# Optimization experiments

Hardware: AMD Instinct MI355X
Metric: run time of the kernel (lower is better)

Reference implementation:

```python
import jax, jax.numpy as jnp
import numpy as np
import math

# ---------- real Clebsch-Gordan coupling tables (computed once, tiny) ----------
def _cg(j1, m1, j2, m2, j3, m3):
    if m1 + m2 != m3 or j3 < abs(j1 - j2) or j3 > j1 + j2:
        return 0.0
    f = math.factorial
    pre = ((2 * j3 + 1) * f(j3 + j1 - j2) * f(j3 - j1 + j2) * f(j1 + j2 - j3) / f(j1 + j2 + j3 + 1)) ** 0.5
    pre *= (f(j3 + m3) * f(j3 - m3) * f(j1 - m1) * f(j1 + m1) * f(j2 - m2) * f(j2 + m2)) ** 0.5
    s = 0.0
    for k in range(0, j1 + j2 - j3 + 1):
        d = (k, j1 + j2 - j3 - k, j1 - m1 - k, j2 + m2 - k, j3 - j2 + m1 + k, j3 - j1 - m2 + k)
        if min(d) < 0:
            continue
        den = 1
        for t in d:
            den *= f(t)
        s += (-1) ** k / den
    return pre * s

def _Q(l):  # complex->real spherical-harmonic change of basis
    Q = np.zeros((2 * l + 1, 2 * l + 1), dtype=complex)
    Q[l, l] = 1.0
    s = 2 ** -0.5
    for m in range(1, l + 1):
        Q[l + m, l + m] = (-1) ** m * s
        Q[l + m, l - m] = s
        Q[l - m, l + m] = -1j * (-1) ** m * s
        Q[l - m, l - m] = 1j * s
    return Q

def _K(l1, l2, l3):  # real coupling tensor [2l3+1, 2l1+1, 2l2+1]
    C = np.zeros((2 * l3 + 1, 2 * l1 + 1, 2 * l2 + 1), dtype=complex)
    for M3 in range(-l3, l3 + 1):
        for M1 in range(-l1, l1 + 1):
            for M2 in range(-l2, l2 + 1):
                C[M3 + l3, M1 + l1, M2 + l2] = _cg(l1, M1, l2, M2, l3, M3)
    K = np.einsum('cC,aA,bB,CAB->cab', _Q(l3).conj(), _Q(l1), _Q(l2), C)
    K = K.imag if np.abs(K.imag).max() > np.abs(K.real).max() else K.real
    return np.asarray(K, dtype=np.float32)

# the 9 'uvu' instructions (in_l, edge_l, out_l) with multiplicities (weight_numel=144)
_PATHS = [(0, 0, 0), (0, 2, 2), (1, 0, 1), (1, 2, 1), (1, 2, 2), (2, 0, 2), (2, 2, 0), (2, 2, 1), (2, 2, 2)]
_KT = [jnp.asarray(_K(*p)) for p in _PATHS]
_MULS = [32, 32, 16, 16, 16, 8, 8, 8, 8]
_SPLITS = np.cumsum(_MULS)[:-1].tolist()
NEI = 8
EPS = 1e-5

def _sh(u):  # component-normalized real SH of unit vectors, l=0..2 (m order -l..l, l=1 -> y,z,x)
    x, y, z = u[:, 0], u[:, 1], u[:, 2]
    sh0 = jnp.ones_like(x)[:, None]
    sh1 = np.float32(3 ** 0.5) * jnp.stack([y, z, x], -1)
    s15 = np.float32(15 ** 0.5)
    s5 = np.float32(5 ** 0.5)
    sh2 = jnp.stack([s15 * x * y, s15 * y * z, 0.5 * s5 * (3 * z * z - 1.0), s15 * x * z, 0.5 * s15 * (x * x - y * y)], -1)
    return sh0, sh1, sh2

def _path(xs, sh, wp, Kt):  # xs [E,u,2l1+1], sh [E,2l2+1], Kt [2l3+1,2l1+1,2l2+1] -> [E,u,2l3+1]
    return jnp.einsum('eui,ej,oij->euo', xs, sh, Kt) * wp[None, :, None]

def _layer(x0, x1, x2, pos, src, dst, w, W0, W1, W2, bw0, bb0, bw1, bw2, N):
    ev = pos[dst] - pos[src]
    u = ev / (jnp.linalg.norm(ev, axis=1, keepdims=True) + 1e-12)
    sh0, sh1, sh2 = _sh(u)
    s0 = x0[src][:, :, None]  # [E,32,1]
    s1 = x1[src]              # [E,16,3]
    s2 = x2[src]              # [E,8,5]
    ws = jnp.split(w, _SPLITS)
    p1 = _path(s0, sh0, ws[0], _KT[0])
    p2 = _path(s0, sh2, ws[1], _KT[1])
    p3 = _path(s1, sh0, ws[2], _KT[2])
    p4 = _path(s1, sh2, ws[3], _KT[3])
    p5 = _path(s1, sh2, ws[4], _KT[4])
    p6 = _path(s2, sh0, ws[5], _KT[5])
    p7 = _path(s2, sh2, ws[6], _KT[6])
    p8 = _path(s2, sh2, ws[7], _KT[7])
    p9 = _path(s2, sh2, ws[8], _KT[8])
    m0 = jnp.concatenate([p1, p7], 1)          # [E,40,1]
    m1 = jnp.concatenate([p3, p4, p8], 1)      # [E,40,3]
    m2 = jnp.concatenate([p2, p5, p6, p9], 1)  # [E,64,5]
    a0 = jax.ops.segment_sum(m0, dst, num_segments=N)
    a1 = jax.ops.segment_sum(m1, dst, num_segments=N)
    a2 = jax.ops.segment_sum(m2, dst, num_segments=N)
    y0 = (a0[:, :, 0] @ W0) * np.float32(1.0 / 40 ** 0.5)
    y1 = jnp.einsum('num,uv->nvm', a1, W1) * np.float32(1.0 / 40 ** 0.5)
    y2 = jnp.einsum('num,uv->nvm', a2, W2) * np.float32(1.0 / 64 ** 0.5)
    # equivariant batchnorm (training stats): scalars -> standard BN, l>0 -> norm BN
    f = y0 - y0.mean(0)
    y0 = f / jnp.sqrt((f * f).mean(0) + EPS) * bw0 + bb0
    y1 = y1 / jnp.sqrt((y1 * y1).mean(axis=(0, 2)) + EPS)[None, :, None] * bw1[None, :, None]
    y2 = y2 / jnp.sqrt((y2 * y2).mean(axis=(0, 2)) + EPS)[None, :, None] * bw2[None, :, None]
    return y0, y1, y2

def _forward(positions, W_emb, tp_w, lin_W0, lin_W1, lin_W2, bn_w0, bn_b0, bn_w1, bn_w2, Wf1, Wf2, bf2, Wf3, bf3):
    B, P, _ = positions.shape
    N = B * P
    pos = positions.reshape(N, 3)
    # kNN graph from dense cdist + topk (indices are not differentiated)
    pg = jax.lax.stop_gradient(pos)
    sq = jnp.sum(pg * pg, 1)
    d2 = sq[:, None] + sq[None, :] - 2.0 * (pg @ pg.T)
    _, idx = jax.lax.top_k(-d2, NEI + 1)  # smallest distances; col 0 is self
    src = jnp.repeat(jnp.arange(N), NEI)
    dst = idx[:, 1:].reshape(-1)
    x0 = jnp.ones((N, 1), jnp.float32) @ W_emb  # embedding: only 0e->0e path exists
    x1 = jnp.zeros((N, 16, 3), jnp.float32)
    x2 = jnp.zeros((N, 8, 5), jnp.float32)
    for l in range(3):
        y0, y1, y2 = _layer(x0, x1, x2, pos, src, dst, tp_w[l], lin_W0[l], lin_W1[l], lin_W2[l],
                            bn_w0[l], bn_b0[l], bn_w1[l], bn_w2[l], N)
        x0 = jax.nn.relu(y0) + x0
        x1 = jax.nn.relu(y1) + x1
        x2 = jax.nn.relu(y2) + x2
    h = jax.nn.relu((x0 @ Wf1) * np.float32(1.0 / 32 ** 0.5))  # scalar part -> 32x0e
    h = jax.nn.relu(h @ Wf2 + bf2)
    out = (h @ Wf3 + bf3).reshape(B, P, 2)
    return out

def setup_inputs() -> dict:
    key = jax.random.key(0)
    ks = jax.random.split(key, 16)
    B, P = 4, 2048
    return {
        'positions': jax.random.normal(ks[0], (B, P, 3), jnp.float32) * 3.0,
        'W_emb': jax.random.normal(ks[1], (1, 32), jnp.float32),
        'tp_w': jax.random.normal(ks[2], (3, 144), jnp.float32),
        'lin_W0': jax.random.normal(ks[3], (3, 40, 32), jnp.float32),
        'lin_W1': jax.random.normal(ks[4], (3, 40, 16), jnp.float32),
        'lin_W2': jax.random.normal(ks[5], (3, 64, 8), jnp.float32),
        'bn_w0': 1.0 + 0.05 * jax.random.normal(ks[6], (3, 32), jnp.float32),
        'bn_b0': jnp.zeros((3, 32), jnp.float32),
        'bn_w1': 1.0 + 0.05 * jax.random.normal(ks[7], (3, 16), jnp.float32),
        'bn_w2': 1.0 + 0.05 * jax.random.normal(ks[8], (3, 8), jnp.float32),
        'Wf1': jax.random.normal(ks[9], (32, 32), jnp.float32),
        'Wf2': jax.random.normal(ks[10], (32, 16), jnp.float32) * 0.2,
        'bf2': jax.random.normal(ks[11], (16,), jnp.float32) * 0.1,
        'Wf3': jax.random.normal(ks[12], (16, 2), jnp.float32) * 0.2,
        'bf3': jax.random.normal(ks[13], (2,), jnp.float32) * 0.1,
    }

def reference(positions, W_emb, tp_w, lin_W0, lin_W1, lin_W2, bn_w0, bn_b0, bn_w1, bn_w2, Wf1, Wf2, bf2, Wf3, bf3):
    return _forward(positions, W_emb, tp_w, lin_W0, lin_W1, lin_W2, bn_w0, bn_b0, bn_w1, bn_w2, Wf1, Wf2, bf2, Wf3, bf3)
```

## Files before the change

kernel.cpp:

```cpp
#include <hip/hip_runtime.h>
#include <math.h>

#define NN 8192
#define REV_CAP 48
#define KNN_CAP 384
#define PF 12

static const size_t OFF_K     = 0;
static const size_t OFF_CNT   = 512;
static const size_t OFF_REV   = 8704;
static const size_t OFF_STATS = 401920;
static const size_t OFF_XF    = 406528;
static const size_t OFF_YF    = 1389568;
static const size_t WS_FLOATS = 2372608;

__device__ double dfact(int n){ double r=1.0; for(int i=2;i<=n;++i) r*=(double)i; return r; }

__device__ double dcg(int j1,int m1,int j2,int m2,int j3,int m3){
  if (m1+m2!=m3) return 0.0;
  if (j3 < abs(j1-j2) || j3 > j1+j2) return 0.0;
  double pre = sqrt((double)(2*j3+1)*dfact(j3+j1-j2)*dfact(j3-j1+j2)*dfact(j1+j2-j3)/dfact(j1+j2+j3+1));
  pre *= sqrt(dfact(j3+m3)*dfact(j3-m3)*dfact(j1-m1)*dfact(j1+m1)*dfact(j2-m2)*dfact(j2+m2));
  double s=0.0;
  for(int k=0;k<=j1+j2-j3;++k){
    int d1=j1+j2-j3-k, d2=j1-m1-k, d3=j2+m2-k, d4=j3-j2+m1+k, d5=j3-j1-m2+k;
    if(d1<0||d2<0||d3<0||d4<0||d5<0) continue;
    double den = dfact(k)*dfact(d1)*dfact(d2)*dfact(d3)*dfact(d4)*dfact(d5);
    s += ((k&1)? -1.0: 1.0)/den;
  }
  return pre*s;
}

__device__ int qrow(int l,int r,int* col,double* re,double* im){
  const double s = 0.70710678118654752440;
  if (r==l){ col[0]=l; re[0]=1.0; im[0]=0.0; return 1; }
  if (r>l){ int m=r-l;
    col[0]=l+m; re[0]=((m&1)?-s:s); im[0]=0.0;
    col[1]=l-m; re[1]=s;            im[1]=0.0;
  } else { int m=l-r;
    col[0]=l+m; re[0]=0.0; im[0]=((m&1)? s : -s);
    col[1]=l-m; re[1]=0.0; im[1]=s;
  }
  return 2;
}

__global__ __launch_bounds__(256) void k_setup(const float* __restrict__ pos,
        const float* __restrict__ W_emb, float* __restrict__ Kbuf,
        float* __restrict__ xf,
        float* __restrict__ xs, float* __restrict__ ys, float* __restrict__ zs,
        float* __restrict__ qs,
        int* __restrict__ cnt){
  int idx = blockIdx.x*256 + threadIdx.x;
  if (idx < 983040) { const int c = idx%120; xf[idx] = (c<32)? W_emb[c] : 0.f; return; }
  idx -= 983040;
  if (idx < 8192) {
    const float x=pos[3*idx], y=pos[3*idx+1], z=pos[3*idx+2];
    xs[idx]=x; ys[idx]=y; zs[idx]=z; qs[idx]=0.5f*(x*x+y*y+z*z);
    return;
  }
  idx -= 8192;
  if (idx < 8192) { cnt[idx]=0; return; }
  idx -= 8192;
  if (idx >= 405) return;

  const int tid = idx;
  const int sizes[9]={1,25,9,45,75,25,25,75,125};
  const int l1s[9]={0,0,1,1,1,2,2,2,2};
  const int l2s[9]={0,2,0,2,2,0,2,2,2};
  const int l3s[9]={0,2,1,1,2,2,0,1,2};
  int p=0, rem=tid;
  for(p=0;p<9;++p){ if(rem < sizes[p]) break; rem -= sizes[p]; }
  const int l1=l1s[p], l2=l2s[p], l3=l3s[p];
  const int n1=2*l1+1, n2=2*l2+1;
  const int c = rem/(n1*n2); const int r2 = rem%(n1*n2); const int a=r2/n2; const int b=r2%n2;

  int c3[2],c1[2],c2[2]; double re3[2],im3[2],re1[2],im1[2],re2[2],im2[2];
  const int nc3 = qrow(l3,c,c3,re3,im3);
  const int nc1 = qrow(l1,a,c1,re1,im1);
  const int nc2 = qrow(l2,b,c2,re2,im2);

  double accRe=0, accIm=0;
  for(int i3=0;i3<nc3;++i3){
    const double q3re=re3[i3], q3im=-im3[i3];
    for(int i1=0;i1<nc1;++i1){
      const double pre_re = q3re*re1[i1] - q3im*im1[i1];
      const double pre_im = q3re*im1[i1] + q3im*re1[i1];
      for(int i2=0;i2<nc2;++i2){
        const double cgv = dcg(l1, c1[i1]-l1, l2, c2[i2]-l2, l3, c3[i3]-l3);
        if (cgv==0.0) continue;
        accRe += (pre_re*re2[i2] - pre_im*im2[i2])*cgv;
        accIm += (pre_re*im2[i2] + pre_im*re2[i2])*cgv;
      }
    }
  }
  const bool useImag = ((l1+l2+l3)&1)!=0;
  Kbuf[tid] = (float)(useImag? accIm : accRe);
}

__global__ __launch_bounds__(256) void k_knn8(const float* __restrict__ xs,
                                              const float* __restrict__ ys,
                                              const float* __restrict__ zs,
                                              const float* __restrict__ qs,
                                              int* __restrict__ cnt, int* __restrict__ rev){
  const int lane = threadIdx.x & 63;
  const int w    = threadIdx.x >> 6;
  const int node = blockIdx.x*4 + w;
  __shared__ float sdist[4][KNN_CAP];
  __shared__ int   sidx[4][KNN_CAP];
  __shared__ int   scount[4];
  if (threadIdx.x < 4) scount[threadIdx.x]=0;
  __syncthreads();

  const float px = xs[node], py = ys[node], pz = zs[node];

  float m1 = INFINITY, m2 = INFINITY;
  for(int c=0;c<4;++c){
    const int base = (c*64 + lane)*4;
    const float4 fx = *(const float4*)(xs + base);
    const float4 fy = *(const float4*)(ys + base);
    const float4 fz = *(const float4*)(zs + base);
    const float4 fq = *(const float4*)(qs + base);
    float ss[4];
    ss[0] = fmaf(-px,fx.x, fmaf(-py,fy.x, fmaf(-pz,fz.x, fq.x)));
    ss[1] = fmaf(-px,fx.y, fmaf(-py,fy.y, fmaf(-pz,fz.y, fq.y)));
    ss[2] = fmaf(-px,fx.z, fmaf(-py,fy.z, fmaf(-pz,fz.z, fq.z)));
    ss[3] = fmaf(-px,fx.w, fmaf(-py,fy.w, fmaf(-pz,fz.w, fq.w)));
    #pragma unroll
    for(int q=0;q<4;++q){
      const float hi = fmaxf(m1, ss[q]);
      m1 = fminf(m1, ss[q]);
      m2 = fminf(m2, hi);
    }
  }
  float T = INFINITY;
  for(int r=0;r<9;++r){
    float v = m1; int l = lane;
    #pragma unroll
    for(int s=32;s>0;s>>=1){
      const float ov=__shfl_xor(v,s,64); const int ol=__shfl_xor(l,s,64);
      if (ov<v || (ov==v && ol<l)){ v=ov; l=ol; }
    }
    T = v;
    if (lane==l){ m1=m2; m2=INFINITY; }
  }

  for(int c=0;c<32;++c){
    const int base = (c*64 + lane)*4;
    const float4 fx = *(const float4*)(xs + base);
    const float4 fy = *(const float4*)(ys + base);
    const float4 fz = *(const float4*)(zs + base);
    const float4 fq = *(const float4*)(qs + base);
    float ss[4];
    ss[0] = fmaf(-px,fx.x, fmaf(-py,fy.x, fmaf(-pz,fz.x, fq.x)));
    ss[1] = fmaf(-px,fx.y, fmaf(-py,fy.y, fmaf(-pz,fz.y, fq.y)));
    ss[2] = fmaf(-px,fx.z, fmaf(-py,fy.z, fmaf(-pz,fz.z, fq.z)));
    ss[3] = fmaf(-px,fx.w, fmaf(-py,fy.w, fmaf(-pz,fz.w, fq.w)));
    #pragma unroll
    for(int q=0;q<4;++q){
      if (ss[q] <= T){
        int pos = atomicAdd(&scount[w],1);
        if (pos < KNN_CAP){ sdist[w][pos]=ss[q]; sidx[w][pos]=base+q; }
      }
    }
  }
  __syncthreads();

  int m = scount[w]; if (m > KNN_CAP) m = KNN_CAP;
  float dl[KNN_CAP/64]; int il[KNN_CAP/64];
  #pragma unroll
  for(int k=0;k<KNN_CAP/64;++k){
    const int j = lane + 64*k;
    if (j < m){ dl[k]=sdist[w][j]; il[k]=sidx[w][j]; }
    else      { dl[k]=INFINITY;    il[k]=0x7fffffff; }
  }
  for(int r=0;r<9;++r){
    float bv=dl[0]; int bi=il[0];
    #pragma unroll
    for(int k=1;k<KNN_CAP/64;++k){
      if (dl[k]<bv || (dl[k]==bv && il[k]<bi)){ bv=dl[k]; bi=il[k]; }
    }
    float v=bv; int ix=bi;
    #pragma unroll
    for(int s=32;s>0;s>>=1){
      float ov=__shfl_xor(v,s,64); int oi=__shfl_xor(ix,s,64);
      if (ov<v || (ov==v && oi<ix)){ v=ov; ix=oi; }
    }
    if (ix != node && lane==0){
      int cpos = atomicAdd(&cnt[ix],1);
      if (cpos < REV_CAP) rev[ix*REV_CAP + cpos] = node;
    }
    #pragma unroll
    for(int k=0;k<KNN_CAP/64;++k){
      if (il[k]==ix){ dl[k]=INFINITY; il[k]=0x7fffffff; }
    }
  }
}

__global__ __launch_bounds__(256) void k_msg(
  const float* __restrict__ pos,
  const int* __restrict__ cnt, const int* __restrict__ rev,
  const float* __restrict__ Kbuf,
  const float* __restrict__ xf,
  const float* __restrict__ tpw,
  const float* __restrict__ W0, const float* __restrict__ W1, const float* __restrict__ W2,
  float* __restrict__ yf)
{
  const int t = threadIdx.x;
  const int w = t >> 6;
  const int lane = t & 63;
  const int n = blockIdx.x*4 + w;

  __shared__ float KL[405];
  __shared__ float TW[144];
  __shared__ float momP[4][120];
  __shared__ float momS[4][600];
  __shared__ float aS[4][480];
  __shared__ int   eIdx[4][REV_CAP];
  __shared__ float eSh[4][5][REV_CAP];
  for(int q=t;q<405;q+=256) KL[q]=Kbuf[q];
  for(int q=t;q<144;q+=256) TW[q]=tpw[q];

  const int deg0 = cnt[n];
  const int deg = (deg0<REV_CAP)? deg0 : REV_CAP;
  const float pnx=pos[3*n], pny=pos[3*n+1], pnz=pos[3*n+2];
  const float s15 = 3.8729833462f, s5c = 2.2360679775f;
  if (lane < deg){
    const int i = rev[n*REV_CAP+lane];
    eIdx[w][lane] = i;
    const float ex = pnx - pos[3*i], ey = pny - pos[3*i+1], ez = pnz - pos[3*i+2];
    const float rn = sqrtf(ex*ex+ey*ey+ez*ez) + 1e-12f;
    const float ux=ex/rn, uy=ey/rn, uz=ez/rn;
    eSh[w][0][lane]=s15*ux*uy;
    eSh[w][1][lane]=s15*uy*uz;
    eSh[w][2][lane]=0.5f*s5c*(3.f*uz*uz-1.f);
    eSh[w][3][lane]=s15*ux*uz;
    eSh[w][4][lane]=0.5f*s15*(ux*ux-uy*uy);
  }
  __syncthreads();

  const int c0 = lane*2;
  float mp0=0.f, mp1=0.f;
  float ms0[5], ms1[5];
  #pragma unroll
  for(int j=0;j<5;++j){ ms0[j]=0.f; ms1[j]=0.f; }

  int idxr[PF];
  #pragma unroll
  for(int k=0;k<PF;++k) idxr[k] = (k<deg)? eIdx[w][k] : 0;
  float2 fr[PF];
  if (lane<60){
    #pragma unroll
    for(int k=0;k<PF;++k) fr[k] = *(const float2*)(xf + (size_t)idxr[k]*120 + c0);
  }
  #pragma unroll
  for(int k=0;k<PF;++k){
    if (k<deg){
      const float sh0=eSh[w][0][k], sh1=eSh[w][1][k], sh2=eSh[w][2][k];
      const float sh3=eSh[w][3][k], sh4=eSh[w][4][k];
      if (lane<60){
        const float2 f = fr[k];
        mp0 += f.x; mp1 += f.y;
        ms0[0]+=f.x*sh0; ms0[1]+=f.x*sh1; ms0[2]+=f.x*sh2; ms0[3]+=f.x*sh3; ms0[4]+=f.x*sh4;
        ms1[0]+=f.y*sh0; ms1[1]+=f.y*sh1; ms1[2]+=f.y*sh2; ms1[3]+=f.y*sh3; ms1[4]+=f.y*sh4;
      }
    }
  }
  for(int e=PF;e<deg;++e){
    const int i = eIdx[w][e];
    const float sh0=eSh[w][0][e], sh1=eSh[w][1][e], sh2=eSh[w][2][e];
    const float sh3=eSh[w][3][e], sh4=eSh[w][4][e];
    if (lane<60){
      const float2 f = *(const float2*)(xf + (size_t)i*120 + c0);
      mp0 += f.x; mp1 += f.y;
      ms0[0]+=f.x*sh0; ms0[1]+=f.x*sh1; ms0[2]+=f.x*sh2; ms0[3]+=f.x*sh3; ms0[4]+=f.x*sh4;
      ms1[0]+=f.y*sh0; ms1[1]+=f.y*sh1; ms1[2]+=f.y*sh2; ms1[3]+=f.y*sh3; ms1[4]+=f.y*sh4;
    }
  }
  if (lane<60){
    momP[w][c0]=mp0; momP[w][c0+1]=mp1;
    #pragma unroll
    for(int j=0;j<5;++j){ momS[w][c0*5+j]=ms0[j]; momS[w][(c0+1)*5+j]=ms1[j]; }
  }
  __syncthreads();

  float acc[14];
  #pragma unroll
  for(int k=0;k<14;++k) acc[k]=0.f;

  if (lane<32){
    const int u=lane;
    const float rw0=TW[u], rw1=TW[32+u];
    acc[0] = rw0 * KL[0] * momP[w][u];
    float m0s[5];
    #pragma unroll
    for(int j=0;j<5;++j) m0s[j]=momS[w][u*5+j];
    #pragma unroll
    for(int o=0;o<5;++o){ float g=0.f;
      #pragma unroll
      for(int j=0;j<5;++j) g += KL[1+o*5+j]*m0s[j];
      acc[1+o] = rw1*g; }
  } else if (lane<48){
    const int u=lane-32;
    const float rw0=TW[64+u], rw1=TW[80+u], rw2=TW[96+u];
    float m1p[3], m1s[3][5];
    #pragma unroll
    for(int i=0;i<3;++i){
      m1p[i]=momP[w][32+u*3+i];
      #pragma unroll
      for(int j=0;j<5;++j) m1s[i][j]=momS[w][(32+u*3+i)*5+j];
    }
    #pragma unroll
    for(int o=0;o<3;++o){ float g=0.f;
      #pragma unroll
      for(int i=0;i<3;++i) g += KL[26+o*3+i]*m1p[i];
      acc[o]=rw0*g; }
    #pragma unroll
    for(int o=0;o<3;++o){ float g=0.f;
      #pragma unroll
      for(int i=0;i<3;++i)
        #pragma unroll
        for(int j=0;j<5;++j) g += KL[35+(o*3+i)*5+j]*m1s[i][j];
      acc[3+o]=rw1*g; }
    #pragma unroll
    for(int o=0;o<5;++o){ float g=0.f;
      #pragma unroll
      for(int i=0;i<3;++i)
        #pragma unroll
        for(int j=0;j<5;++j) g += KL[80+(o*3+i)*5+j]*m1s[i][j];
      acc[6+o]=rw2*g; }
  } else if (lane<56){
    const int u=lane-48;
    const float rw0=TW[112+u], rw1=TW[120+u], rw2=TW[128+u], rw3=TW[136+u];
    float m2p[5], m2s[5][5];
    #pragma unroll
    for(int i=0;i<5;++i){
      m2p[i]=momP[w][80+u*5+i];
      #pragma unroll
      for(int j=0;j<5;++j) m2s[i][j]=momS[w][(80+u*5+i)*5+j];
    }
    #pragma unroll
    for(int o=0;o<5;++o){ float g=0.f;
      #pragma unroll
      for(int i=0;i<5;++i) g += KL[155+o*5+i]*m2p[i];
      acc[o]=rw0*g; }
    { float g=0.f;
      #pragma unroll
      for(int i=0;i<5;++i)
        #pragma unroll
        for(int j=0;j<5;++j) g += KL[180+i*5+j]*m2s[i][j];
      acc[5]=rw1*g; }
    #pragma unroll
    for(int o=0;o<3;++o){ float g=0.f;
      #pragma unroll
      for(int i=0;i<5;++i)
        #pragma unroll
        for(int j=0;j<5;++j) g += KL[205+(o*5+i)*5+j]*m2s[i][j];
      acc[6+o]=rw2*g; }
    #pragma unroll
    for(int o=0;o<5;++o){ float g=0.f;
      #pragma unroll
      for(int i=0;i<5;++i)
        #pragma unroll
        for(int j=0;j<5;++j) g += KL[280+(o*5+i)*5+j]*m2s[i][j];
      acc[9+o]=rw3*g; }
  }

  if (lane<32){
    aS[w][lane] = acc[0];
    #pragma unroll
    for(int o=0;o<5;++o) aS[w][160 + lane*5+o] = acc[1+o];
  } else if (lane<48){
    const int uu=lane-32;
    #pragma unroll
    for(int m=0;m<3;++m){ aS[w][40 + uu*3+m] = acc[m]; aS[w][40 + (16+uu)*3+m] = acc[3+m]; }
    #pragma unroll
    for(int o=0;o<5;++o) aS[w][160 + (32+uu)*5+o] = acc[6+o];
  } else if (lane<56){
    const int uu=lane-48;
    aS[w][32+uu] = acc[5];
    #pragma unroll
    for(int m=0;m<3;++m) aS[w][40 + (32+uu)*3+m] = acc[6+m];
    #pragma unroll
    for(int o=0;o<5;++o){ aS[w][160 + (48+uu)*5+o] = acc[o]; aS[w][160 + (56+uu)*5+o] = acc[9+o]; }
  }
  __syncthreads();

  const float inv40 = 0.15811388300841896660f;
  for(int q=lane;q<120;q+=64){
    float out;
    if (q<32){
      float g=0.f;
      for(int uu=0;uu<40;++uu) g += aS[w][uu]*W0[uu*32+q];
      out = g*inv40;
    } else if (q<80){
      const int e=q-32, v=e/3, m=e%3;
      float g=0.f;
      for(int uu=0;uu<40;++uu) g += aS[w][40+uu*3+m]*W1[uu*16+v];
      out = g*inv40;
    } else {
      const int e=q-80, tt=e/5, m=e%5;
      float g=0.f;
      for(int uu=0;uu<64;++uu) g += aS[w][160+uu*5+m]*W2[uu*8+tt];
      out = g*0.125f;
    }
    yf[(size_t)n*120+q] = out;
  }
}

__global__ __launch_bounds__(256) void k_statp(const float* __restrict__ yf,
                                               float* __restrict__ pA, float* __restrict__ pB){
  const int ch = blockIdx.x % 96;
  const int chunk = blockIdx.x / 96;
  const int t = threadIdx.x;
  const int n0 = chunk*1024;
  __shared__ float r1[256], r2[256];
  float a1=0.f, a2=0.f;
  if (ch<32){
    for(int nn=t;nn<1024;nn+=256){ float v=yf[(size_t)(n0+nn)*120+ch]; a1+=v; a2+=v*v; }
  } else if (ch<48){
    const int v_=ch-32;
    for(int nn=t;nn<1024;nn+=256){
      #pragma unroll
      for(int m=0;m<3;++m){ float v=yf[(size_t)(n0+nn)*120+32+v_*3+m]; a2+=v*v; }
    }
  } else {
    const int t_=ch-48;
    for(int nn=t;nn<1024;nn+=256){
      #pragma unroll
      for(int m=0;m<5;++m){ float v=yf[(size_t)(n0+nn)*120+80+t_*5+m]; a2+=v*v; }
    }
  }
  r1[t]=a1; r2[t]=a2; __syncthreads();
  for(int s=128;s>0;s>>=1){ if(t<s){ r1[t]+=r1[t+s]; r2[t]+=r2[t+s]; } __syncthreads(); }
  if(t==0){ pA[ch*8+chunk]=r1[0]; pB[ch*8+chunk]=r2[0]; }
}

__global__ __launch_bounds__(256) void k_norm(const float* __restrict__ yf,
                       const float* __restrict__ pA, const float* __restrict__ pB,
                       const float* __restrict__ bw0,const float* __restrict__ bb0,
                       const float* __restrict__ bw1,const float* __restrict__ bw2,
                       float* __restrict__ xf){
  __shared__ float sc[96], sf[32];
  const int t = threadIdx.x;
  if (t<96){
    float sB=0.f;
    #pragma unroll
    for(int k=0;k<8;++k) sB += pB[t*8+k];
    float scale;
    if (t<32){
      float sA=0.f;
      #pragma unroll
      for(int k=0;k<8;++k) sA += pA[t*8+k];
      const float mean = sA*(1.f/8192.f);
      const float var  = sB*(1.f/8192.f) - mean*mean;
      const float inv  = 1.f/sqrtf(var+1e-5f);
      scale = bw0[t]*inv;
      sf[t] = bb0[t] - mean*scale;
    } else if (t<48){
      scale = bw1[t-32]/sqrtf(sB*(1.f/(8192.f*3.f))+1e-5f);
    } else {
      scale = bw2[t-48]/sqrtf(sB*(1.f/(8192.f*5.f))+1e-5f);
    }
    sc[t]=scale;
  }
  __syncthreads();
  const int idx = blockIdx.x*256 + t;
  if (idx >= NN*120) return;
  const int c = idx%120;
  const int chan = (c<32)? c : ((c<80)? 32+(c-32)/3 : 48+(c-80)/5);
  const float v = yf[idx]*sc[chan] + ((c<32)? sf[c] : 0.f);
  xf[idx] += fmaxf(v,0.f);
}

__global__ __launch_bounds__(256) void k_normmlp(const float* __restrict__ yf,
                                             const float* __restrict__ xf,
                                             const float* __restrict__ pA, const float* __restrict__ pB,
                                             const float* __restrict__ bw0,const float* __restrict__ bb0,
                                             const float* __restrict__ Wf1,const float* __restrict__ Wf2,
                                             const float* __restrict__ bf2,const float* __restrict__ Wf3,
                                             const float* __restrict__ bf3, float* __restrict__ out){
  __shared__ float w1[1024], w2[512], w3[32], b2[16], b3[2], sc0[32], sf0[32];
  const int t=threadIdx.x;
  for(int q=t;q<1024;q+=256) w1[q]=Wf1[q];
  for(int q=t;q<512;q+=256)  w2[q]=Wf2[q];
  if(t<32) w3[t]=Wf3[t];
  if(t<16) b2[t]=bf2[t];
  if(t<2)  b3[t]=bf3[t];
  if(t<32){
    float sA=0.f, sB=0.f;
    #pragma unroll
    for(int k=0;k<8;++k){ sA += pA[t*8+k]; sB += pB[t*8+k]; }
    const float mean = sA*(1.f/8192.f);
    const float var  = sB*(1.f/8192.f) - mean*mean;
    const float inv  = 1.f/sqrtf(var+1e-5f);
    sc0[t] = bw0[t]*inv;
    sf0[t] = bb0[t] - mean*sc0[t];
  }
  __syncthreads();
  const int n = blockIdx.x*256+t;
  if(n>=NN) return;
  float xv[32];
  #pragma unroll
  for(int k=0;k<32;++k){
    const float v = yf[(size_t)n*120+k]*sc0[k] + sf0[k];
    xv[k] = xf[(size_t)n*120+k] + fmaxf(v,0.f);
  }
  const float inv32 = 0.17677669529663688110f;
  float h1[32];
  #pragma unroll 4
  for(int c=0;c<32;++c){ float g=0.f;
    #pragma unroll
    for(int k=0;k<32;++k) g+=xv[k]*w1[k*32+c];
    h1[c]=fmaxf(g*inv32,0.f); }
  float h2[16];
  #pragma unroll 4
  for(int c=0;c<16;++c){ float g=b2[c];
    #pragma unroll
    for(int k=0;k<32;++k) g+=h1[k]*w2[k*16+c];
    h2[c]=fmaxf(g,0.f); }
  #pragma unroll
  for(int m=0;m<2;++m){ float g=b3[m];
    #pragma unroll
    for(int k=0;k<16;++k) g+=h2[k]*w3[k*2+m];
    out[n*2+m]=g; }
}

extern "C" void kernel_launch(void* const* d_in, const int* in_sizes, int n_in,
                              void* d_out, int out_size, void* d_ws, size_t ws_size,
                              hipStream_t stream) {
  const float* positions = (const float*)d_in[0];
  const float* W_emb  = (const float*)d_in[1];
  const float* tp_w   = (const float*)d_in[2];
  const float* lin_W0 = (const float*)d_in[3];
  const float* lin_W1 = (const float*)d_in[4];
  const float* lin_W2 = (const float*)d_in[5];
  const float* bn_w0  = (const float*)d_in[6];
  const float* bn_b0  = (const float*)d_in[7];
  const float* bn_w1  = (const float*)d_in[8];
  const float* bn_w2  = (const float*)d_in[9];
  const float* Wf1 = (const float*)d_in[10];
  const float* Wf2 = (const float*)d_in[11];
  const float* bf2 = (const float*)d_in[12];
  const float* Wf3 = (const float*)d_in[13];
  const float* bf3 = (const float*)d_in[14];

  if (ws_size < WS_FLOATS*sizeof(float)) return;

  float* ws    = (float*)d_ws;
  float* Kbuf  = ws + OFF_K;
  int*   cnt   = (int*)(ws + OFF_CNT);
  int*   rev   = (int*)(ws + OFF_REV);
  float* stats = ws + OFF_STATS;
  float* xf = ws + OFF_XF;
  float* yf = ws + OFF_YF;

  float* xs = yf;
  float* ysA = yf + NN;
  float* zs = yf + 2*NN;
  float* qs = yf + 3*NN;

  k_setup<<<3906,256,0,stream>>>(positions, W_emb, Kbuf, xf, xs, ysA, zs, qs, cnt);
  k_knn8<<<NN/4,256,0,stream>>>(xs, ysA, zs, qs, cnt, rev);

  for(int l=0;l<3;++l){
    float* pA = stats + l*1536;
    float* pB = pA + 768;
    k_msg<<<NN/4,256,0,stream>>>(positions, cnt, rev, Kbuf, xf,
                              tp_w + l*144, lin_W0 + l*40*32, lin_W1 + l*40*16, lin_W2 + l*64*8,
                              yf);
    k_statp<<<768,256,0,stream>>>(yf, pA, pB);
    if (l<2){
      k_norm<<<(NN*120+255)/256,256,0,stream>>>(yf, pA, pB,
                              bn_w0 + l*32, bn_b0 + l*32, bn_w1 + l*16, bn_w2 + l*8,
                              xf);
    }
  }
  k_normmlp<<<NN/256,256,0,stream>>>(yf, xf, stats + 2*1536, stats + 2*1536 + 768,
                              bn_w0 + 64, bn_b0 + 64,
                              Wf1, Wf2, bf2, Wf3, bf3, (float*)d_out);
}
```

Baseline: 297.6 us.

## Process four query nodes per wavefront in kNN to reuse candidate loads

Each wavefront in the kNN kernel now handles four query nodes instead of one, so every float4 load of the candidate coordinates is reused across four distance computations. Shared memory stores only candidate indices, and distances are recomputed from global memory during the final selection, which reduces LDS footprint. The grid shrinks by four times, which lowers parallelism to 512 blocks and raises register pressure, and the per-node threshold and selection phases run sequentially.

```diff
diff --git a/kernel.cpp b/kernel.cpp
--- a/kernel.cpp
+++ b/kernel.cpp
@@ -104,44 +104,56 @@
                                               int* __restrict__ cnt, int* __restrict__ rev){
   const int lane = threadIdx.x & 63;
   const int w    = threadIdx.x >> 6;
-  const int node = blockIdx.x*4 + w;
-  __shared__ float sdist[4][KNN_CAP];
-  __shared__ int   sidx[4][KNN_CAP];
-  __shared__ int   scount[4];
-  if (threadIdx.x < 4) scount[threadIdx.x]=0;
+  const int nb   = blockIdx.x*16 + w*4;
+  __shared__ int sidx[16][KNN_CAP];
+  __shared__ int scount[16];
+  if (threadIdx.x < 16) scount[threadIdx.x]=0;
   __syncthreads();
 
-  const float px = xs[node], py = ys[node], pz = zs[node];
-
-  float m1 = INFINITY, m2 = INFINITY;
+  float px[4], py[4], pz[4];
+  #pragma unroll
+  for(int u=0;u<4;++u){ px[u]=xs[nb+u]; py[u]=ys[nb+u]; pz[u]=zs[nb+u]; }
+
+  float m1[4], m2[4];
+  #pragma unroll
+  for(int u=0;u<4;++u){ m1[u]=INFINITY; m2[u]=INFINITY; }
   for(int c=0;c<4;++c){
     const int base = (c*64 + lane)*4;
     const float4 fx = *(const float4*)(xs + base);
     const float4 fy = *(const float4*)(ys + base);
     const float4 fz = *(const float4*)(zs + base);
     const float4 fq = *(const float4*)(qs + base);
-    float ss[4];
-    ss[0] = fmaf(-px,fx.x, fmaf(-py,fy.x, fmaf(-pz,fz.x, fq.x)));
-    ss[1] = fmaf(-px,fx.y, fmaf(-py,fy.y, fmaf(-pz,fz.y, fq.y)));
-    ss[2] = fmaf(-px,fx.z, fmaf(-py,fy.z, fmaf(-pz,fz.z, fq.z)));
-    ss[3] = fmaf(-px,fx.w, fmaf(-py,fy.w, fmaf(-pz,fz.w, fq.w)));
+    const float cx[4]={fx.x,fx.y,fx.z,fx.w};
+    const float cy[4]={fy.x,fy.y,fy.z,fy.w};
+    const float cz[4]={fz.x,fz.y,fz.z,fz.w};
+    const float cq[4]={fq.x,fq.y,fq.z,fq.w};
     #pragma unroll
     for(int q=0;q<4;++q){
-      const float hi = fmaxf(m1, ss[q]);
-      m1 = fminf(m1, ss[q]);
-      m2 = fminf(m2, hi);
-    }
-  }
-  float T = INFINITY;
-  for(int r=0;r<9;++r){
-    float v = m1; int l = lane;
-    #pragma unroll
-    for(int s=32;s>0;s>>=1){
-      const float ov=__shfl_xor(v,s,64); const int ol=__shfl_xor(l,s,64);
-      if (ov<v || (ov==v && ol<l)){ v=ov; l=ol; }
-    }
-    T = v;
-    if (lane==l){ m1=m2; m2=INFINITY; }
+      #pragma unroll
+      for(int u=0;u<4;++u){
+        const float s  = fmaf(-px[u],cx[q], fmaf(-py[u],cy[q], fmaf(-pz[u],cz[q], cq[q])));
+        const float hi = fmaxf(m1[u], s);
+        m1[u] = fminf(m1[u], s);
+        m2[u] = fminf(m2[u], hi);
+      }
+    }
+  }
+  float T[4];
+  #pragma unroll 1
+  for(int u=0;u<4;++u){
+    float a1=m1[u], a2=m2[u];
+    float Tu=INFINITY;
+    for(int r=0;r<9;++r){
+      float v = a1; int l = lane;
+      #pragma unroll
+      for(int s=32;s>0;s>>=1){
+        const float ov=__shfl_xor(v,s,64); const int ol=__shfl_xor(l,s,64);
+        if (ov<v || (ov==v && ol<l)){ v=ov; l=ol; }
+      }
+      Tu = v;
+      if (lane==l){ a1=a2; a2=INFINITY; }
+    }
+    T[u]=Tu;
   }
 
   for(int c=0;c<32;++c){
@@ -150,48 +162,58 @@
     const float4 fy = *(const float4*)(ys + base);
     const float4 fz = *(const float4*)(zs + base);
     const float4 fq = *(const float4*)(qs + base);
-    float ss[4];
-    ss[0] = fmaf(-px,fx.x, fmaf(-py,fy.x, fmaf(-pz,fz.x, fq.x)));
-    ss[1] = fmaf(-px,fx.y, fmaf(-py,fy.y, fmaf(-pz,fz.y, fq.y)));
-    ss[2] = fmaf(-px,fx.z, fmaf(-py,fy.z, fmaf(-pz,fz.z, fq.z)));
-    ss[3] = fmaf(-px,fx.w, fmaf(-py,fy.w, fmaf(-pz,fz.w, fq.w)));
+    const float cx[4]={fx.x,fx.y,fx.z,fx.w};
+    const float cy[4]={fy.x,fy.y,fy.z,fy.w};
+    const float cz[4]={fz.x,fz.y,fz.z,fz.w};
+    const float cq[4]={fq.x,fq.y,fq.z,fq.w};
     #pragma unroll
     for(int q=0;q<4;++q){
-      if (ss[q] <= T){
-        int pos = atomicAdd(&scount[w],1);
-        if (pos < KNN_CAP){ sdist[w][pos]=ss[q]; sidx[w][pos]=base+q; }
+      #pragma unroll
+      for(int u=0;u<4;++u){
+        const float s = fmaf(-px[u],cx[q], fmaf(-py[u],cy[q], fmaf(-pz[u],cz[q], cq[q])));
+        if (s <= T[u]){
+          int pos = atomicAdd(&scount[w*4+u],1);
+          if (pos < KNN_CAP) sidx[w*4+u][pos] = base+q;
+        }
       }
     }
   }
   __syncthreads();
 
-  int m = scount[w]; if (m > KNN_CAP) m = KNN_CAP;
-  float dl[KNN_CAP/64]; int il[KNN_CAP/64];
-  #pragma unroll
-  for(int k=0;k<KNN_CAP/64;++k){
-    const int j = lane + 64*k;
-    if (j < m){ dl[k]=sdist[w][j]; il[k]=sidx[w][j]; }
-    else      { dl[k]=INFINITY;    il[k]=0x7fffffff; }
-  }
-  for(int r=0;r<9;++r){
-    float bv=dl[0]; int bi=il[0];
-    #pragma unroll
-    for(int k=1;k<KNN_CAP/64;++k){
-      if (dl[k]<bv || (dl[k]==bv && il[k]<bi)){ bv=dl[k]; bi=il[k]; }
-    }
-    float v=bv; int ix=bi;
-    #pragma unroll
-    for(int s=32;s>0;s>>=1){
-      float ov=__shfl_xor(v,s,64); int oi=__shfl_xor(ix,s,64);
-      if (ov<v || (ov==v && oi<ix)){ v=ov; ix=oi; }
-    }
-    if (ix != node && lane==0){
-      int cpos = atomicAdd(&cnt[ix],1);
-      if (cpos < REV_CAP) rev[ix*REV_CAP + cpos] = node;
-    }
+  #pragma unroll 1
+  for(int u=0;u<4;++u){
+    const int node = nb+u;
+    int m = scount[w*4+u]; if (m > KNN_CAP) m = KNN_CAP;
+    float dl[KNN_CAP/64]; int il[KNN_CAP/64];
     #pragma unroll
     for(int k=0;k<KNN_CAP/64;++k){
-      if (il[k]==ix){ dl[k]=INFINITY; il[k]=0x7fffffff; }
+      const int j = lane + 64*k;
+      if (j < m){
+        const int id = sidx[w*4+u][j];
+        il[k]=id;
+        dl[k]=fmaf(-px[u],xs[id], fmaf(-py[u],ys[id], fmaf(-pz[u],zs[id], qs[id])));
+      } else { dl[k]=INFINITY; il[k]=0x7fffffff; }
+    }
+    for(int r=0;r<9;++r){
+      float bv=dl[0]; int bi=il[0];
+      #pragma unroll
+      for(int k=1;k<KNN_CAP/64;++k){
+        if (dl[k]<bv || (dl[k]==bv && il[k]<bi)){ bv=dl[k]; bi=il[k]; }
+      }
+      float v=bv; int ix=bi;
+      #pragma unroll
+      for(int s=32;s>0;s>>=1){
+        float ov=__shfl_xor(v,s,64); int oi=__shfl_xor(ix,s,64);
+        if (ov<v || (ov==v && oi<ix)){ v=ov; ix=oi; }
+      }
+      if (ix != node && lane==0){
+        int cpos = atomicAdd(&cnt[ix],1);
+        if (cpos < REV_CAP) rev[ix*REV_CAP + cpos] = node;
+      }
+      #pragma unroll
+      for(int k=0;k<KNN_CAP/64;++k){
+        if (il[k]==ix){ dl[k]=INFINITY; il[k]=0x7fffffff; }
+      }
     }
   }
 }
@@ -560,7 +582,7 @@
   float* qs = yf + 3*NN;
 
   k_setup<<<3906,256,0,stream>>>(positions, W_emb, Kbuf, xf, xs, ysA, zs, qs, cnt);
-  k_knn8<<<NN/4,256,0,stream>>>(xs, ysA, zs, qs, cnt, rev);
+  k_knn8<<<NN/16,256,0,stream>>>(xs, ysA, zs, qs, cnt, rev);
 
   for(int l=0;l<3;++l){
     float* pA = stats + l*1536;
```

Result: slower. 339.1 us (+14.0%).

## Stage KNN candidate coordinates through double-buffered shared-memory tiles

Applied to the files above, without the earlier changes.

The KNN kernel previously had each wave read the x/y/z/q arrays straight from global memory, once for the threshold pass and again for the full scan. Now the whole block cooperatively loads 512-point tiles into double-buffered LDS, prefetching the next tile into registers while the current one is processed, so the four waves share each global load. The cost is one barrier per tile plus 16KB of extra LDS, which may lower occupancy. The block-wide barriers also now sit on the path where lanes branch to do atomic inserts.

```diff
diff --git a/kernel.cpp b/kernel.cpp
--- a/kernel.cpp
+++ b/kernel.cpp
@@ -5,6 +5,8 @@
 #define REV_CAP 48
 #define KNN_CAP 384
 #define PF 12
+#define TS 512
+#define NTILE 16
 
 static const size_t OFF_K     = 0;
 static const size_t OFF_CNT   = 512;
@@ -102,65 +104,88 @@
                                               const float* __restrict__ zs,
                                               const float* __restrict__ qs,
                                               int* __restrict__ cnt, int* __restrict__ rev){
-  const int lane = threadIdx.x & 63;
-  const int w    = threadIdx.x >> 6;
+  const int t256 = threadIdx.x;
+  const int lane = t256 & 63;
+  const int w    = t256 >> 6;
   const int node = blockIdx.x*4 + w;
+  __shared__ float tile[2][4*TS];
   __shared__ float sdist[4][KNN_CAP];
   __shared__ int   sidx[4][KNN_CAP];
   __shared__ int   scount[4];
-  if (threadIdx.x < 4) scount[threadIdx.x]=0;
-  __syncthreads();
+  if (t256 < 4) scount[t256]=0;
 
   const float px = xs[node], py = ys[node], pz = zs[node];
 
+  const int seg = t256 >> 7;
+  const int sub = t256 & 127;
+  const float* g0 = seg ? ys : xs;
+  const float* g1 = seg ? qs : zs;
+
   float m1 = INFINITY, m2 = INFINITY;
-  for(int c=0;c<4;++c){
-    const int base = (c*64 + lane)*4;
-    const float4 fx = *(const float4*)(xs + base);
-    const float4 fy = *(const float4*)(ys + base);
-    const float4 fz = *(const float4*)(zs + base);
-    const float4 fq = *(const float4*)(qs + base);
-    float ss[4];
-    ss[0] = fmaf(-px,fx.x, fmaf(-py,fy.x, fmaf(-pz,fz.x, fq.x)));
-    ss[1] = fmaf(-px,fx.y, fmaf(-py,fy.y, fmaf(-pz,fz.y, fq.y)));
-    ss[2] = fmaf(-px,fx.z, fmaf(-py,fy.z, fmaf(-pz,fz.z, fq.z)));
-    ss[3] = fmaf(-px,fx.w, fmaf(-py,fy.w, fmaf(-pz,fz.w, fq.w)));
-    #pragma unroll
-    for(int q=0;q<4;++q){
-      const float hi = fmaxf(m1, ss[q]);
-      m1 = fminf(m1, ss[q]);
-      m2 = fminf(m2, hi);
-    }
-  }
-  float T = INFINITY;
-  for(int r=0;r<9;++r){
-    float v = m1; int l = lane;
-    #pragma unroll
-    for(int s=32;s>0;s>>=1){
-      const float ov=__shfl_xor(v,s,64); const int ol=__shfl_xor(l,s,64);
-      if (ov<v || (ov==v && ol<l)){ v=ov; l=ol; }
-    }
-    T = v;
-    if (lane==l){ m1=m2; m2=INFINITY; }
-  }
-
-  for(int c=0;c<32;++c){
-    const int base = (c*64 + lane)*4;
-    const float4 fx = *(const float4*)(xs + base);
-    const float4 fy = *(const float4*)(ys + base);
-    const float4 fz = *(const float4*)(zs + base);
-    const float4 fq = *(const float4*)(qs + base);
-    float ss[4];
-    ss[0] = fmaf(-px,fx.x, fmaf(-py,fy.x, fmaf(-pz,fz.x, fq.x)));
-    ss[1] = fmaf(-px,fx.y, fmaf(-py,fy.y, fmaf(-pz,fz.y, fq.y)));
-    ss[2] = fmaf(-px,fx.z, fmaf(-py,fy.z, fmaf(-pz,fz.z, fq.z)));
-    ss[3] = fmaf(-px,fx.w, fmaf(-py,fy.w, fmaf(-pz,fz.w, fq.w)));
-    #pragma unroll
-    for(int q=0;q<4;++q){
-      if (ss[q] <= T){
-        int pos = atomicAdd(&scount[w],1);
-        if (pos < KNN_CAP){ sdist[w][pos]=ss[q]; sidx[w][pos]=base+q; }
+  float T  = INFINITY;
+
+  float4 r0 = *(const float4*)(g0 + sub*4);
+  float4 r1 = *(const float4*)(g1 + sub*4);
+  *(float4*)(&tile[0][       seg*TS + sub*4]) = r0;
+  *(float4*)(&tile[0][2*TS + seg*TS + sub*4]) = r1;
+  int cur = 0;
+
+  for (int v = 0; v < NTILE+2; ++v){
+    const int vn = v+1;
+    if (vn < NTILE+2){
+      const int tn = (vn<2)? vn : vn-2;
+      r0 = *(const float4*)(g0 + tn*TS + sub*4);
+      r1 = *(const float4*)(g1 + tn*TS + sub*4);
+    }
+    __syncthreads();
+    const float* tb = tile[cur];
+    const int tt = (v<2)? v : v-2;
+    #pragma unroll
+    for (int qq=0; qq<TS/256; ++qq){
+      const int fo = (qq*64+lane)*4;
+      const float4 fx = *(const float4*)(tb + fo);
+      const float4 fy = *(const float4*)(tb +   TS + fo);
+      const float4 fz = *(const float4*)(tb + 2*TS + fo);
+      const float4 fq = *(const float4*)(tb + 3*TS + fo);
+      float ss[4];
+      ss[0] = fmaf(-px,fx.x, fmaf(-py,fy.x, fmaf(-pz,fz.x, fq.x)));
+      ss[1] = fmaf(-px,fx.y, fmaf(-py,fy.y, fmaf(-pz,fz.y, fq.y)));
+      ss[2] = fmaf(-px,fx.z, fmaf(-py,fy.z, fmaf(-pz,fz.z, fq.z)));
+      ss[3] = fmaf(-px,fx.w, fmaf(-py,fy.w, fmaf(-pz,fz.w, fq.w)));
+      if (v < 2){
+        #pragma unroll
+        for(int q=0;q<4;++q){
+          const float hi = fmaxf(m1, ss[q]);
+          m1 = fminf(m1, ss[q]);
+          m2 = fminf(m2, hi);
+        }
+      } else {
+        #pragma unroll
+        for(int q=0;q<4;++q){
+          if (ss[q] <= T){
+            int pos = atomicAdd(&scount[w],1);
+            if (pos < KNN_CAP){ sdist[w][pos]=ss[q]; sidx[w][pos]=tt*TS + fo + q; }
+          }
+        }
       }
+    }
+    if (v == 1){
+      for(int r=0;r<9;++r){
+        float rv = m1; int rl = lane;
+        #pragma unroll
+        for(int s=32;s>0;s>>=1){
+          const float ov=__shfl_xor(rv,s,64); const int ol=__shfl_xor(rl,s,64);
+          if (ov<rv || (ov==rv && ol<rl)){ rv=ov; rl=ol; }
+        }
+        T = rv;
+        if (lane==rl){ m1=m2; m2=INFINITY; }
+      }
+    }
+    if (vn < NTILE+2){
+      float* db = tile[cur^1];
+      *(float4*)(db +        seg*TS + sub*4) = r0;
+      *(float4*)(db + 2*TS + seg*TS + sub*4) = r1;
+      cur ^= 1;
     }
   }
   __syncthreads();
```

New measurement: 307.9 us. 1.03x slower.

## Replace iterative shuffle-argmin kNN selection with ballot-based radix select

Applied to the files above, without the earlier changes.

The kNN kernel's threshold search and final top-9 selection used to run 9 rounds of wavefront shuffle-argmin reductions. Both now use a 32-step bitwise radix select on order-preserving float keys, counting candidates with ballot and popcount. Ties at the threshold are broken by a small extra loop over indices. This cuts shuffle traffic and serial dependency but adds 32 ballot iterations, and the output order of the atomic reverse-list writes changes.

```diff
diff --git a/kernel.cpp b/kernel.cpp
--- a/kernel.cpp
+++ b/kernel.cpp
@@ -97,6 +97,11 @@
   Kbuf[tid] = (float)(useImag? accIm : accRe);
 }
 
+__device__ __forceinline__ unsigned fkey(float f){
+  const unsigned b = __float_as_uint(f);
+  return (b & 0x80000000u) ? ~b : (b | 0x80000000u);
+}
+
 __global__ __launch_bounds__(256) void k_knn8(const float* __restrict__ xs,
                                               const float* __restrict__ ys,
                                               const float* __restrict__ zs,
@@ -132,17 +137,18 @@
       m2 = fminf(m2, hi);
     }
   }
-  float T = INFINITY;
-  for(int r=0;r<9;++r){
-    float v = m1; int l = lane;
-    #pragma unroll
-    for(int s=32;s>0;s>>=1){
-      const float ov=__shfl_xor(v,s,64); const int ol=__shfl_xor(l,s,64);
-      if (ov<v || (ov==v && ol<l)){ v=ov; l=ol; }
-    }
-    T = v;
-    if (lane==l){ m1=m2; m2=INFINITY; }
-  }
+  {
+    const unsigned kk1 = fkey(m1), kk2 = fkey(m2);
+    unsigned P = 0u; int need = 9;
+    #pragma unroll 1
+    for(int bit=31; bit>=0; --bit){
+      const unsigned pref = P >> bit;
+      const int c0 = __popcll(__ballot((kk1>>bit)==pref)) + __popcll(__ballot((kk2>>bit)==pref));
+      if (need > c0){ need -= c0; P |= (1u<<bit); }
+    }
+    m1 = __uint_as_float((P & 0x80000000u) ? (P & 0x7fffffffu) : ~P);
+  }
+  const float T = m1;
 
   for(int c=0;c<32;++c){
     const int base = (c*64 + lane)*4;
@@ -166,32 +172,48 @@
   __syncthreads();
 
   int m = scount[w]; if (m > KNN_CAP) m = KNN_CAP;
-  float dl[KNN_CAP/64]; int il[KNN_CAP/64];
+  unsigned ku[KNN_CAP/64]; int il[KNN_CAP/64];
   #pragma unroll
   for(int k=0;k<KNN_CAP/64;++k){
     const int j = lane + 64*k;
-    if (j < m){ dl[k]=sdist[w][j]; il[k]=sidx[w][j]; }
-    else      { dl[k]=INFINITY;    il[k]=0x7fffffff; }
-  }
-  for(int r=0;r<9;++r){
-    float bv=dl[0]; int bi=il[0];
-    #pragma unroll
-    for(int k=1;k<KNN_CAP/64;++k){
-      if (dl[k]<bv || (dl[k]==bv && il[k]<bi)){ bv=dl[k]; bi=il[k]; }
-    }
-    float v=bv; int ix=bi;
-    #pragma unroll
-    for(int s=32;s>0;s>>=1){
-      float ov=__shfl_xor(v,s,64); int oi=__shfl_xor(ix,s,64);
-      if (ov<v || (ov==v && oi<ix)){ v=ov; ix=oi; }
-    }
-    if (ix != node && lane==0){
+    if (j < m){ ku[k]=fkey(sdist[w][j]); il[k]=sidx[w][j]; }
+    else      { ku[k]=0xffffffffu;       il[k]=0x7fffffff; }
+  }
+  unsigned P = 0u; int need = 9;
+  #pragma unroll 1
+  for(int bit=31; bit>=0; --bit){
+    const unsigned pref = P >> bit;
+    int c0 = 0;
+    #pragma unroll
+    for(int k=0;k<KNN_CAP/64;++k) c0 += __popcll(__ballot((ku[k]>>bit)==pref));
+    if (need > c0){ need -= c0; P |= (1u<<bit); }
+  }
+  int c_eq = 0;
+  #pragma unroll
+  for(int k=0;k<KNN_CAP/64;++k) c_eq += __popcll(__ballot(ku[k]==P));
+  bool tsel[KNN_CAP/64];
+  #pragma unroll
+  for(int k=0;k<KNN_CAP/64;++k) tsel[k] = (ku[k]==P);
+  if (c_eq > need){
+    #pragma unroll
+    for(int k=0;k<KNN_CAP/64;++k) tsel[k]=false;
+    for(int r=0;r<need;++r){
+      int mid = 0x7fffffff;
+      #pragma unroll
+      for(int k=0;k<KNN_CAP/64;++k) if (ku[k]==P && !tsel[k] && il[k]<mid) mid = il[k];
+      #pragma unroll
+      for(int s=32;s>0;s>>=1){ const int om = __shfl_xor(mid,s,64); mid = (om<mid)? om : mid; }
+      #pragma unroll
+      for(int k=0;k<KNN_CAP/64;++k) if (ku[k]==P && il[k]==mid) tsel[k]=true;
+    }
+  }
+  #pragma unroll
+  for(int k=0;k<KNN_CAP/64;++k){
+    const bool take = (ku[k] < P) || tsel[k];
+    const int ix = il[k];
+    if (take && ix != node){
       int cpos = atomicAdd(&cnt[ix],1);
       if (cpos < REV_CAP) rev[ix*REV_CAP + cpos] = node;
-    }
-    #pragma unroll
-    for(int k=0;k<KNN_CAP/64;++k){
-      if (il[k]==ix){ dl[k]=INFINITY; il[k]=0x7fffffff; }
     }
   }
 }
```

After: 293.6 us. No clear change (-1.3%).
